# Performance work log

Hardware: AMD Instinct MI355X
Metric: run time of the kernel (lower is better)

## Reference

```python
import jax, jax.numpy as jnp
import numpy as np

NUM_GROUPS = 32
EPS = 1e-6


def setup_inputs() -> dict:
    key = jax.random.key(0)
    ks = jax.random.split(key, 6)
    b, c, H, W = 4, 512, 64, 64
    scale = 1.0 / np.sqrt(c)
    return {
        "x": jax.random.normal(ks[0], (b, c, H, W), dtype=jnp.float32),
        "gn_w": jnp.ones((c,), jnp.float32),
        "gn_b": jnp.zeros((c,), jnp.float32),
        "wq": jax.random.normal(ks[1], (c, c), jnp.float32) * scale,
        "bq": jnp.zeros((c,), jnp.float32),
        "wk": jax.random.normal(ks[2], (c, c), jnp.float32) * scale,
        "bk": jnp.zeros((c,), jnp.float32),
        "wv": jax.random.normal(ks[3], (c, c), jnp.float32) * scale,
        "bv": jnp.zeros((c,), jnp.float32),
        "wp": jax.random.normal(ks[4], (c, c), jnp.float32) * scale,
        "bp": jnp.zeros((c,), jnp.float32),
    }


def _group_norm(x, gamma, beta):
    b, c, H, W = x.shape
    xg = x.reshape(b, NUM_GROUPS, c // NUM_GROUPS, H, W)
    mean = xg.mean(axis=(2, 3, 4), keepdims=True)
    var = xg.var(axis=(2, 3, 4), keepdims=True)
    xn = (xg - mean) * jax.lax.rsqrt(var + EPS)
    xn = xn.reshape(b, c, H, W)
    return xn * gamma[None, :, None, None] + beta[None, :, None, None]


def reference(x, gn_w, gn_b, wq, bq, wk, bk, wv, bv, wp, bp):
    b, c, H, W = x.shape
    h = _group_norm(x, gn_w, gn_b)  # (b,c,H,W)
    hf = h.reshape(b, c, H * W)  # (b,c,n)
    # 1x1 convs == per-pixel linear maps; weight layout [out,in]
    q = jnp.einsum('oc,bcn->bno', wq, hf) + bq  # (b,n,c)
    k = jnp.einsum('oc,bcn->bon', wk, hf) + bk[None, :, None]  # (b,c,n)
    v = jnp.einsum('oc,bcn->bon', wv, hf) + bv[None, :, None]  # (b,c,n)
    attn = jnp.einsum('bnc,bcm->bnm', q, k) * (int(c) ** (-0.5))
    attn = jax.nn.softmax(attn, axis=2)  # softmax over keys m
    # A = v @ attn^T  -> (b,c,n) where A[:, :, n] = sum_m v[:,:,m] attn[n,m]
    A = jnp.einsum('bcm,bnm->bcn', v, attn)
    A = jnp.einsum('oc,bcn->bon', wp, A) + bp[None, :, None]
    return x + A.reshape(b, c, H, W)
```

## Files before the change

kernel.cpp:

```cpp
#include <hip/hip_runtime.h>

#define BATCH 4
#define CCH 512
#define NPIX 4096
#define NGRP 32
#define GSZ 16
#define GN_EPS 1e-6f

typedef __attribute__((ext_vector_type(8))) short short8;
typedef __attribute__((ext_vector_type(8))) unsigned short ushort8;
typedef __attribute__((ext_vector_type(4))) unsigned short ushort4v;
typedef __attribute__((ext_vector_type(4))) float f32x4;

__device__ inline unsigned short f2bf(float f) {
  unsigned u = __float_as_uint(f);
  unsigned r = u + 0x7fffu + ((u >> 16) & 1u);
  return (unsigned short)(r >> 16);
}
__device__ inline float bf2f(unsigned short us) {
  return __uint_as_float(((unsigned)us) << 16);
}

__global__ __launch_bounds__(256) void gn_stats(const float* __restrict__ x,
                                                float* __restrict__ stats) {
  int bg = blockIdx.x;
  const f32x4* base = (const f32x4*)(x + (size_t)bg * (GSZ * NPIX));
  float s = 0.f, ss = 0.f;
  const int n4 = GSZ * NPIX / 4;
  for (int i = threadIdx.x; i < n4; i += 256) {
    f32x4 v = base[i];
    s += v.x + v.y + v.z + v.w;
    ss += v.x * v.x + v.y * v.y + v.z * v.z + v.w * v.w;
  }
  for (int off = 32; off > 0; off >>= 1) {
    s += __shfl_xor(s, off, 64);
    ss += __shfl_xor(ss, off, 64);
  }
  __shared__ float rs[4], rss[4];
  int lane = threadIdx.x & 63, wid = threadIdx.x >> 6;
  if (lane == 0) { rs[wid] = s; rss[wid] = ss; }
  __syncthreads();
  if (threadIdx.x == 0) {
    float S = rs[0] + rs[1] + rs[2] + rs[3];
    float SS = rss[0] + rss[1] + rss[2] + rss[3];
    const float inv = 1.f / (float)(GSZ * NPIX);
    float mean = S * inv;
    float var = SS * inv - mean * mean;
    stats[bg * 2] = mean;
    stats[bg * 2 + 1] = rsqrtf(var + GN_EPS);
  }
}

__global__ __launch_bounds__(256) void gn_apply_t(const float* __restrict__ x,
                                                  const float* __restrict__ stats,
                                                  const float* __restrict__ gw,
                                                  const float* __restrict__ gb,
                                                  unsigned short* __restrict__ hT) {
  __shared__ float tile[64][65];
  int b = blockIdx.z, c0 = blockIdx.y * 64, n0 = blockIdx.x * 64;
  int t = threadIdx.x;
  int tc4 = t & 15, tr = t >> 4;
  const float* xb = x + ((size_t)b * CCH + c0) * NPIX + n0;
#pragma unroll
  for (int j = 0; j < 4; ++j) {
    int row = tr + j * 16;
    int c = c0 + row;
    float mean = stats[((size_t)b * NGRP + (c >> 4)) * 2];
    float rstd = stats[((size_t)b * NGRP + (c >> 4)) * 2 + 1];
    float ga = gw[c] * rstd;
    float be = gb[c] - mean * ga;
    f32x4 v = *(const f32x4*)(xb + (size_t)row * NPIX + tc4 * 4);
    tile[row][tc4 * 4 + 0] = v.x * ga + be;
    tile[row][tc4 * 4 + 1] = v.y * ga + be;
    tile[row][tc4 * 4 + 2] = v.z * ga + be;
    tile[row][tc4 * 4 + 3] = v.w * ga + be;
  }
  __syncthreads();
  int cc = t & 7, nr = t >> 3;
  unsigned short* outp = hT + ((size_t)b * NPIX + n0) * CCH + c0;
#pragma unroll
  for (int j = 0; j < 2; ++j) {
    int n = nr + j * 32;
    ushort8 pk;
#pragma unroll
    for (int i = 0; i < 8; ++i) pk[i] = f2bf(tile[cc * 8 + i][n]);
    *(ushort8*)(outp + (size_t)n * CCH + cc * 8) = pk;
  }
}

__global__ __launch_bounds__(256) void f32_to_bf16(const float* __restrict__ src,
                                                   unsigned short* __restrict__ dst,
                                                   int n4) {
  int i = blockIdx.x * 256 + threadIdx.x;
  if (i < n4) {
    f32x4 v = ((const f32x4*)src)[i];
    ushort4v o;
    o.x = f2bf(v.x); o.y = f2bf(v.y); o.z = f2bf(v.z); o.w = f2bf(v.w);
    ((ushort4v*)dst)[i] = o;
  }
}

template <int BIAS_MODE, int OUT_BF16, int RESID, int SWZ>
__global__ __launch_bounds__(256, 2) void gemm_bt(
    const unsigned short* __restrict__ A, const unsigned short* __restrict__ B,
    void* __restrict__ Cv, const float* __restrict__ bias,
    const float* __restrict__ resid, int M, int N, int K, int lda, int ldb,
    int ldc, long sA, long sB, long sC, long sR, float scale) {
  __shared__ __align__(16) unsigned short lA[128][40];
  __shared__ __align__(16) unsigned short lB[128][40];
  const int t = threadIdx.x;
  const int lane = t & 63, w = t >> 6;
  const int wr = w >> 1, wc = w & 1;
  const int fr = lane & 15, kg = lane >> 4;

  unsigned orig = blockIdx.x + gridDim.x * (blockIdx.y + gridDim.y * blockIdx.z);
  unsigned nwg = gridDim.x * gridDim.y * gridDim.z;
  unsigned tid = (orig & 7) * (nwg >> 3) + (orig >> 3);
  int mt, ntl, bz;
  if (SWZ == 2) {
    unsigned bx = tid % gridDim.x, r = tid / gridDim.x;
    ntl = (int)bx;
    mt = (int)(r % gridDim.y);
    bz = (int)(r / gridDim.y);
  } else {
    unsigned bx = tid % gridDim.x, r = tid / gridDim.x;
    mt = (int)bx;
    ntl = (int)(r % gridDim.y);
    bz = (int)(r / gridDim.y);
  }
  const int m0 = mt * 128, n0 = ntl * 128;

  const unsigned short* Abz = A + (long)bz * sA;
  const unsigned short* Bbz = B + (long)bz * sB;
  const int srow = t >> 1, skc = (t & 1) * 16;
  const unsigned short* gA = Abz + (size_t)(m0 + srow) * lda + skc;
  const unsigned short* gB = Bbz + (size_t)(n0 + srow) * ldb + skc;

  short8 a0X = *(const short8*)(gA);
  short8 a1X = *(const short8*)(gA + 8);
  short8 b0X = *(const short8*)(gB);
  short8 b1X = *(const short8*)(gB + 8);
  short8 a0Y = *(const short8*)(gA + 32);
  short8 a1Y = *(const short8*)(gA + 40);
  short8 b0Y = *(const short8*)(gB + 32);
  short8 b1Y = *(const short8*)(gB + 40);

  f32x4 acc[4][4];
  const f32x4 zero = {0.f, 0.f, 0.f, 0.f};
#pragma unroll
  for (int m = 0; m < 4; ++m)
#pragma unroll
    for (int n = 0; n < 4; ++n) acc[m][n] = zero;

  const int NT = K >> 5;
#define COMPUTE()                                                             \
  do {                                                                        \
    short8 af[4], bfr[4];                                                     \
    _Pragma("unroll") for (int m = 0; m < 4; ++m) af[m] =                     \
        *(const short8*)&lA[wr * 64 + m * 16 + fr][kg * 8];                   \
    _Pragma("unroll") for (int n = 0; n < 4; ++n) bfr[n] =                    \
        *(const short8*)&lB[wc * 64 + n * 16 + fr][kg * 8];                   \
    _Pragma("unroll") for (int m = 0; m < 4; ++m)                             \
        _Pragma("unroll") for (int n = 0; n < 4; ++n) acc[m][n] =             \
            __builtin_amdgcn_mfma_f32_16x16x32_bf16(af[m], bfr[n],            \
                                                    acc[m][n], 0, 0, 0);      \
  } while (0)

  for (int it = 0; it < NT; it += 2) {
    __syncthreads();
    *(short8*)&lA[srow][skc] = a0X;
    *(short8*)&lA[srow][skc + 8] = a1X;
    *(short8*)&lB[srow][skc] = b0X;
    *(short8*)&lB[srow][skc + 8] = b1X;
    if (it + 2 < NT) {
      a0X = *(const short8*)(gA + (it + 2) * 32);
      a1X = *(const short8*)(gA + (it + 2) * 32 + 8);
      b0X = *(const short8*)(gB + (it + 2) * 32);
      b1X = *(const short8*)(gB + (it + 2) * 32 + 8);
    }
    __syncthreads();
    COMPUTE();
    __syncthreads();
    *(short8*)&lA[srow][skc] = a0Y;
    *(short8*)&lA[srow][skc + 8] = a1Y;
    *(short8*)&lB[srow][skc] = b0Y;
    *(short8*)&lB[srow][skc + 8] = b1Y;
    if (it + 3 < NT) {
      a0Y = *(const short8*)(gA + (it + 3) * 32);
      a1Y = *(const short8*)(gA + (it + 3) * 32 + 8);
      b0Y = *(const short8*)(gB + (it + 3) * 32);
      b1Y = *(const short8*)(gB + (it + 3) * 32 + 8);
    }
    __syncthreads();
    COMPUTE();
  }
#undef COMPUTE

  const int rowbase = m0 + wr * 64 + kg * 4;
  const int colbase = n0 + wc * 64 + fr;
#pragma unroll
  for (int m = 0; m < 4; ++m) {
#pragma unroll
    for (int n = 0; n < 4; ++n) {
      int col = colbase + n * 16;
#pragma unroll
      for (int r = 0; r < 4; ++r) {
        int row = rowbase + m * 16 + r;
        float v = acc[m][n][r] * scale;
        if (BIAS_MODE == 1) v += bias[row];
        if (BIAS_MODE == 2) v += bias[col];
        if (RESID) v += resid[(size_t)bz * sR + (size_t)row * ldc + col];
        size_t idx = (size_t)bz * sC + (size_t)row * ldc + col;
        if (OUT_BF16)
          ((unsigned short*)Cv)[idx] = f2bf(v);
        else
          ((float*)Cv)[idx] = v;
      }
    }
  }
}

__global__ __launch_bounds__(512)
__attribute__((amdgpu_waves_per_eu(2, 2))) void attn_fused(
    const unsigned short* __restrict__ qg, const unsigned short* __restrict__ kgl,
    const unsigned short* __restrict__ vg, unsigned short* __restrict__ og,
    float scale) {
  __shared__ __align__(16) unsigned short Qs[64 * 512];
  __shared__ __align__(16) unsigned short Ck[2][256 * 64];
  __shared__ __align__(16) unsigned short Ps[64 * 128];

  const int t = threadIdx.x;
  const int lane = t & 63, w = t >> 6;
  const int fr = lane & 15, kgp = lane >> 4;

  unsigned logical = ((unsigned)blockIdx.x & 7) * 32 + ((unsigned)blockIdx.x >> 3);
  const int bz = (int)(logical >> 6), qt = (int)(logical & 63);
  const size_t BS = (size_t)NPIX * CCH;
  const unsigned short* qb = qg + (size_t)bz * BS + (size_t)qt * 64 * CCH;
  const unsigned short* kb = kgl + (size_t)bz * BS;
  const unsigned short* vb = vg + (size_t)bz * BS;

  const int krow = t >> 1;
  const int khalf = (t & 1) * 32;
  const int kswz = (krow & 7) << 3;

  short8 RX0, RX1, RX2, RX3, RY0, RY1, RY2, RY3;

#define LOADCH(SET, mt2, sub2)                                                \
  do {                                                                        \
    if ((mt2) < 16) {                                                         \
      const unsigned short* g;                                                \
      if ((sub2) < 8)                                                         \
        g = kb + (size_t)((mt2)*256 + krow) * CCH + (sub2)*64 + khalf;        \
      else                                                                    \
        g = vb + (size_t)t * NPIX + (mt2)*256 + ((sub2)-8) * 32;              \
      SET##0 = *(const short8*)(g);                                           \
      SET##1 = *(const short8*)(g + 8);                                       \
      SET##2 = *(const short8*)(g + 16);                                      \
      SET##3 = *(const short8*)(g + 24);                                      \
    }                                                                         \
  } while (0)

#define WRITEK(BUF, SET)                                                      \
  do {                                                                        \
    unsigned short* d = &Ck[BUF][krow * 64];                                  \
    *(short8*)(d + ((khalf + 0) ^ kswz)) = SET##0;                            \
    *(short8*)(d + ((khalf + 8) ^ kswz)) = SET##1;                            \
    *(short8*)(d + ((khalf + 16) ^ kswz)) = SET##2;                           \
    *(short8*)(d + ((khalf + 24) ^ kswz)) = SET##3;                           \
  } while (0)

#define WRITEV(BUF, SET)                                                      \
  do {                                                                        \
    unsigned short* d = &Ck[BUF][t * 8];                                      \
    *(short8*)(d + 0 * 4096) = SET##0;                                        \
    *(short8*)(d + 1 * 4096) = SET##1;                                        \
    *(short8*)(d + 2 * 4096) = SET##2;                                        \
    *(short8*)(d + 3 * 4096) = SET##3;                                        \
  } while (0)

#define PHASE_BAR()                                                           \
  do {                                                                        \
    asm volatile("s_waitcnt lgkmcnt(0)" ::: "memory");                        \
    __builtin_amdgcn_s_barrier();                                             \
    __builtin_amdgcn_sched_barrier(0);                                        \
  } while (0)

  LOADCH(RX, 0, 0);
  LOADCH(RY, 0, 1);
  {
    const int row = t >> 3, c0 = (t & 7) * 64;
    const unsigned short* src = qb + (size_t)row * CCH + c0;
    const int sw = (row & 7) << 3;
#pragma unroll
    for (int i = 0; i < 8; ++i)
      *(short8*)&Qs[row * 512 + ((c0 + i * 8) ^ sw)] = *(const short8*)(src + i * 8);
  }

  f32x4 s_acc[4][2], o_acc[4][4], racc[4];
  const f32x4 zero = {0.f, 0.f, 0.f, 0.f};
#pragma unroll
  for (int i = 0; i < 4; ++i) {
    s_acc[i][0] = zero; s_acc[i][1] = zero; racc[i] = zero;
#pragma unroll
    for (int n = 0; n < 4; ++n) o_acc[i][n] = zero;
  }

#define EXP_HALF(h)                                                           \
  do {                                                                        \
    if ((w >> 2) == (h)) {                                                    \
      _Pragma("unroll") for (int i = 0; i < 4; ++i) {                         \
        f32x4 p0, p1;                                                         \
        _Pragma("unroll") for (int r = 0; r < 4; ++r) {                       \
          p0[r] = __expf(s_acc[i][0][r] * scale);                             \
          p1[r] = __expf(s_acc[i][1][r] * scale);                             \
        }                                                                     \
        f32x4 rs = p0 + p1;                                                   \
        _Pragma("unroll") for (int off = 1; off <= 8; off <<= 1)              \
            _Pragma("unroll") for (int r = 0; r < 4; ++r) rs[r] +=            \
            __shfl_xor(rs[r], off, 64);                                       \
        racc[i] += rs;                                                        \
        _Pragma("unroll") for (int r = 0; r < 4; ++r) {                       \
          int q = i * 16 + kgp * 4 + r;                                       \
          int sw2 = (q & 7) << 3;                                             \
          Ps[q * 128 + (((w & 3) * 32 + fr) ^ sw2)] = f2bf(p0[r]);            \
          Ps[q * 128 + (((w & 3) * 32 + 16 + fr) ^ sw2)] = f2bf(p1[r]);       \
        }                                                                     \
        s_acc[i][0] = zero; s_acc[i][1] = zero;                               \
      }                                                                       \
    }                                                                         \
  } while (0)

  for (int mt = 0; mt < 16; ++mt) {
#pragma unroll
    for (int sub = 0; sub < 8; ++sub) {
      const int buf = sub & 1;
      if (buf == 0) { WRITEK(0, RX); LOADCH(RX, mt, sub + 2); }
      else          { WRITEK(1, RY); LOADCH(RY, mt, sub + 2); }
      PHASE_BAR();
      __builtin_amdgcn_s_setprio(1);
#pragma unroll
      for (int kk = 0; kk < 2; ++kk) {
        short8 a[4], b[2];
#pragma unroll
        for (int i = 0; i < 4; ++i) {
          int q = i * 16 + fr;
          a[i] = *(const short8*)&Qs[q * 512 +
                 ((sub * 64 + kk * 32 + kgp * 8) ^ ((q & 7) << 3))];
        }
#pragma unroll
        for (int n = 0; n < 2; ++n) {
          int ml = w * 32 + n * 16 + fr;
          b[n] = *(const short8*)&Ck[buf][ml * 64 +
                 ((kk * 32 + kgp * 8) ^ ((ml & 7) << 3))];
        }
#pragma unroll
        for (int i = 0; i < 4; ++i) {
          s_acc[i][0] = __builtin_amdgcn_mfma_f32_16x16x32_bf16(a[i], b[0], s_acc[i][0], 0, 0, 0);
          s_acc[i][1] = __builtin_amdgcn_mfma_f32_16x16x32_bf16(a[i], b[1], s_acc[i][1], 0, 0, 0);
        }
      }
      __builtin_amdgcn_s_setprio(0);
    }
    EXP_HALF(0);
#pragma unroll
    for (int vph = 0; vph < 8; ++vph) {
      const int sub = 8 + vph, buf = sub & 1;
      if (vph == 4) {
        PHASE_BAR();
        EXP_HALF(1);
      }
      if (buf == 0) { WRITEV(0, RX); LOADCH(RX, mt + ((sub + 2) >> 4), (sub + 2) & 15); }
      else          { WRITEV(1, RY); LOADCH(RY, mt + ((sub + 2) >> 4), (sub + 2) & 15); }
      PHASE_BAR();
      __builtin_amdgcn_s_setprio(1);
      {
        short8 a[4], b[4];
#pragma unroll
        for (int i = 0; i < 4; ++i) {
          int q = i * 16 + fr;
          a[i] = *(const short8*)&Ps[q * 128 +
                 (((vph & 3) * 32 + kgp * 8) ^ ((q & 7) << 3))];
        }
#pragma unroll
        for (int n = 0; n < 4; ++n) {
          int c = w * 64 + n * 16 + fr;
          b[n] = *(const short8*)&Ck[buf][kgp * 4096 + c * 8];
        }
#pragma unroll
        for (int i = 0; i < 4; ++i)
#pragma unroll
          for (int n = 0; n < 4; ++n)
            o_acc[i][n] = __builtin_amdgcn_mfma_f32_16x16x32_bf16(a[i], b[n], o_acc[i][n], 0, 0, 0);
      }
      __builtin_amdgcn_s_setprio(0);
    }
  }
#undef LOADCH
#undef WRITEK
#undef WRITEV
#undef EXP_HALF

  __syncthreads();
  float* lred = (float*)Ps;
  float* linv = lred + 512;
  if (fr == 0) {
#pragma unroll
    for (int i = 0; i < 4; ++i)
#pragma unroll
      for (int r = 0; r < 4; ++r)
        lred[(i * 16 + kgp * 4 + r) * 8 + w] = racc[i][r];
  }
  __syncthreads();
  if (t < 64) {
    float s = 0.f;
#pragma unroll
    for (int j = 0; j < 8; ++j) s += lred[t * 8 + j];
    linv[t] = 1.f / s;
  }
  __syncthreads();
#pragma unroll
  for (int i = 0; i < 4; ++i) {
    f32x4 li = *(const f32x4*)&linv[i * 16 + kgp * 4];
#pragma unroll
    for (int n = 0; n < 4; ++n) {
#pragma unroll
      for (int r = 0; r < 4; ++r) {
        int q = i * 16 + kgp * 4 + r;
        int col = w * 64 + n * 16 + fr;
        Qs[q * 512 + (col ^ ((q & 7) << 3))] = f2bf(o_acc[i][n][r] * li[r]);
      }
    }
  }
  __syncthreads();
  {
    const int row = t >> 3, c0 = (t & 7) * 64;
    const int sw = (row & 7) << 3;
    unsigned short* dst = og + (size_t)bz * BS + ((size_t)qt * 64 + row) * CCH + c0;
#pragma unroll
    for (int i = 0; i < 8; ++i)
      *(short8*)(dst + i * 8) = *(const short8*)&Qs[row * 512 + ((c0 + i * 8) ^ sw)];
  }
}

extern "C" void kernel_launch(void* const* d_in, const int* in_sizes, int n_in,
                              void* d_out, int out_size, void* d_ws, size_t ws_size,
                              hipStream_t stream) {
  const float* x = (const float*)d_in[0];
  const float* gnw = (const float*)d_in[1];
  const float* gnb = (const float*)d_in[2];
  const float* wq = (const float*)d_in[3];
  const float* bq = (const float*)d_in[4];
  const float* wk = (const float*)d_in[5];
  const float* bk = (const float*)d_in[6];
  const float* wv = (const float*)d_in[7];
  const float* bv = (const float*)d_in[8];
  const float* wp = (const float*)d_in[9];
  const float* bp = (const float*)d_in[10];
  float* out = (float*)d_out;

  const size_t BS = (size_t)NPIX * CCH;

  char* ws = (char*)d_ws;
  float* stats = (float*)ws;
  unsigned short* hT = (unsigned short*)(ws + 1024);
  unsigned short* Abuf = hT;
  unsigned short* qb = hT + BATCH * BS;
  unsigned short* kTb = qb + BATCH * BS;
  unsigned short* vb = kTb + BATCH * BS;
  unsigned short* wqb = vb + BATCH * BS;
  unsigned short* wkb = wqb + CCH * CCH;
  unsigned short* wvb = wkb + CCH * CCH;
  unsigned short* wpb = wvb + CCH * CCH;
  size_t need = (size_t)((char*)(wpb + CCH * CCH) - ws);
  if (ws_size < need) return;

  f32_to_bf16<<<256, 256, 0, stream>>>(wq, wqb, CCH * CCH / 4);
  f32_to_bf16<<<256, 256, 0, stream>>>(wk, wkb, CCH * CCH / 4);
  f32_to_bf16<<<256, 256, 0, stream>>>(wv, wvb, CCH * CCH / 4);
  f32_to_bf16<<<256, 256, 0, stream>>>(wp, wpb, CCH * CCH / 4);

  gn_stats<<<BATCH * NGRP, 256, 0, stream>>>(x, stats);
  gn_apply_t<<<dim3(NPIX / 64, CCH / 64, BATCH), 256, 0, stream>>>(x, stats, gnw,
                                                                   gnb, hT);

  gemm_bt<2, 1, 0, 2><<<dim3(4, 32, BATCH), 256, 0, stream>>>(
      hT, wqb, qb, bq, nullptr, NPIX, CCH, CCH, CCH, CCH, CCH, (long)BS, 0,
      (long)BS, 0, 1.f);
  gemm_bt<2, 1, 0, 2><<<dim3(4, 32, BATCH), 256, 0, stream>>>(
      hT, wkb, kTb, bk, nullptr, NPIX, CCH, CCH, CCH, CCH, CCH, (long)BS, 0,
      (long)BS, 0, 1.f);
  gemm_bt<1, 1, 0, 0><<<dim3(4, 32, BATCH), 256, 0, stream>>>(
      wvb, hT, vb, bv, nullptr, CCH, NPIX, CCH, CCH, CCH, NPIX, 0, (long)BS,
      (long)BS, 0, 1.f);

  const float sscale = 0.044194173824159216f;
  attn_fused<<<BATCH * 64, 512, 0, stream>>>(qb, kTb, vb, Abuf, sscale);

  gemm_bt<1, 0, 1, 0><<<dim3(4, 32, BATCH), 256, 0, stream>>>(
      wpb, Abuf, out, bp, x, CCH, NPIX, CCH, CCH, CCH, NPIX, 0, (long)BS,
      (long)BS, (long)BS, 1.f);
}
```

Baseline: 377.4 us.

## Stream K/V tiles directly into LDS with global_load_lds in attention

Replaces the register-staged K/V loading (global load to VGPRs, then LDS write) with direct global-to-LDS loads via the global_load_lds builtin. The source addresses are permuted so the XOR swizzle is applied at the source, and the double-buffer schedule is rewritten: the next tile is issued before compute and a vmcnt(0) barrier closes each phase. This removes the VGPR staging registers and the LDS store instructions, which may free registers and issue slots. The cost is a full vmcnt wait at every phase end, which can expose load latency, and the placement of the exp/softmax steps changes.

```diff
diff --git a/kernel.cpp b/kernel.cpp
--- a/kernel.cpp
+++ b/kernel.cpp
@@ -20,6 +20,11 @@
 __device__ inline float bf2f(unsigned short us) {
   return __uint_as_float(((unsigned)us) << 16);
 }
+
+#define GLOAD16(g, l)                                                         \
+  __builtin_amdgcn_global_load_lds(                                           \
+      (__attribute__((address_space(1))) void*)(g),                           \
+      (__attribute__((address_space(3))) void*)(l), 16, 0, 0)
 
 __global__ __launch_bounds__(256) void gn_stats(const float* __restrict__ x,
                                                 float* __restrict__ stats) {
@@ -226,7 +231,7 @@
     const unsigned short* __restrict__ vg, unsigned short* __restrict__ og,
     float scale) {
   __shared__ __align__(16) unsigned short Qs[64 * 512];
-  __shared__ __align__(16) unsigned short Ck[2][256 * 64];
+  __shared__ __align__(16) unsigned short Ck[2][16384];
   __shared__ __align__(16) unsigned short Ps[64 * 128];
 
   const int t = threadIdx.x;
@@ -240,54 +245,56 @@
   const unsigned short* kb = kgl + (size_t)bz * BS;
   const unsigned short* vb = vg + (size_t)bz * BS;
 
-  const int krow = t >> 1;
-  const int khalf = (t & 1) * 32;
-  const int kswz = (krow & 7) << 3;
-
-  short8 RX0, RX1, RX2, RX3, RY0, RY1, RY2, RY3;
-
-#define LOADCH(SET, mt2, sub2)                                                \
+  const int ldsE = w * 2048 + lane * 8;
+  const int krow_lo = lane >> 3, kg_src = (lane & 7) ^ (lane >> 3);
+  const unsigned short* kS0 = kb + (size_t)((w * 4 + 0) * 8 + krow_lo) * CCH + kg_src * 8;
+  const unsigned short* kS1 = kb + (size_t)((w * 4 + 1) * 8 + krow_lo) * CCH + kg_src * 8;
+  const unsigned short* kS2 = kb + (size_t)((w * 4 + 2) * 8 + krow_lo) * CCH + kg_src * 8;
+  const unsigned short* kS3 = kb + (size_t)((w * 4 + 3) * 8 + krow_lo) * CCH + kg_src * 8;
+#define VSRC(i) (vb + (size_t)(((w * 4 + (i)) & 7) * 64 + lane) * NPIX + ((w * 4 + (i)) >> 3) * 8)
+  const unsigned short* vS0 = VSRC(0);
+  const unsigned short* vS1 = VSRC(1);
+  const unsigned short* vS2 = VSRC(2);
+  const unsigned short* vS3 = VSRC(3);
+#undef VSRC
+
+#define ISSUE_K(BUF, mt2, sub2)                                               \
   do {                                                                        \
     if ((mt2) < 16) {                                                         \
-      const unsigned short* g;                                                \
-      if ((sub2) < 8)                                                         \
-        g = kb + (size_t)((mt2)*256 + krow) * CCH + (sub2)*64 + khalf;        \
-      else                                                                    \
-        g = vb + (size_t)t * NPIX + (mt2)*256 + ((sub2)-8) * 32;              \
-      SET##0 = *(const short8*)(g);                                           \
-      SET##1 = *(const short8*)(g + 8);                                       \
-      SET##2 = *(const short8*)(g + 16);                                      \
-      SET##3 = *(const short8*)(g + 24);                                      \
+      const long o = (long)(mt2) * (256 * CCH) + (sub2)*64;                   \
+      GLOAD16(kS0 + o, &Ck[BUF][ldsE]);                                       \
+      GLOAD16(kS1 + o, &Ck[BUF][ldsE + 512]);                                 \
+      GLOAD16(kS2 + o, &Ck[BUF][ldsE + 1024]);                                \
+      GLOAD16(kS3 + o, &Ck[BUF][ldsE + 1536]);                                \
     }                                                                         \
   } while (0)
 
-#define WRITEK(BUF, SET)                                                      \
+#define ISSUE_V(BUF, mt2, vs2)                                                \
   do {                                                                        \
-    unsigned short* d = &Ck[BUF][krow * 64];                                  \
-    *(short8*)(d + ((khalf + 0) ^ kswz)) = SET##0;                            \
-    *(short8*)(d + ((khalf + 8) ^ kswz)) = SET##1;                            \
-    *(short8*)(d + ((khalf + 16) ^ kswz)) = SET##2;                           \
-    *(short8*)(d + ((khalf + 24) ^ kswz)) = SET##3;                           \
+    if ((mt2) < 16) {                                                         \
+      const long o = (long)(mt2)*256 + (vs2)*32;                              \
+      GLOAD16(vS0 + o, &Ck[BUF][ldsE]);                                       \
+      GLOAD16(vS1 + o, &Ck[BUF][ldsE + 512]);                                 \
+      GLOAD16(vS2 + o, &Ck[BUF][ldsE + 1024]);                                \
+      GLOAD16(vS3 + o, &Ck[BUF][ldsE + 1536]);                                \
+    }                                                                         \
   } while (0)
 
-#define WRITEV(BUF, SET)                                                      \
-  do {                                                                        \
-    unsigned short* d = &Ck[BUF][t * 8];                                      \
-    *(short8*)(d + 0 * 4096) = SET##0;                                        \
-    *(short8*)(d + 1 * 4096) = SET##1;                                        \
-    *(short8*)(d + 2 * 4096) = SET##2;                                        \
-    *(short8*)(d + 3 * 4096) = SET##3;                                        \
-  } while (0)
-
-#define PHASE_BAR()                                                           \
+#define BAR_LGKM()                                                            \
   do {                                                                        \
     asm volatile("s_waitcnt lgkmcnt(0)" ::: "memory");                        \
     __builtin_amdgcn_s_barrier();                                             \
     __builtin_amdgcn_sched_barrier(0);                                        \
   } while (0)
 
-  LOADCH(RX, 0, 0);
-  LOADCH(RY, 0, 1);
+#define EXIT_BAR()                                                            \
+  do {                                                                        \
+    asm volatile("s_waitcnt vmcnt(0)" ::: "memory");                          \
+    __builtin_amdgcn_s_barrier();                                             \
+    __builtin_amdgcn_sched_barrier(0);                                        \
+  } while (0)
+
+  ISSUE_K(0, 0, 0);
   {
     const int row = t >> 3, c0 = (t & 7) * 64;
     const unsigned short* src = qb + (size_t)row * CCH + c0;
@@ -296,6 +303,7 @@
     for (int i = 0; i < 8; ++i)
       *(short8*)&Qs[row * 512 + ((c0 + i * 8) ^ sw)] = *(const short8*)(src + i * 8);
   }
+  __syncthreads();
 
   f32x4 s_acc[4][2], o_acc[4][4], racc[4];
   const f32x4 zero = {0.f, 0.f, 0.f, 0.f};
@@ -335,9 +343,9 @@
 #pragma unroll
     for (int sub = 0; sub < 8; ++sub) {
       const int buf = sub & 1;
-      if (buf == 0) { WRITEK(0, RX); LOADCH(RX, mt, sub + 2); }
-      else          { WRITEK(1, RY); LOADCH(RY, mt, sub + 2); }
-      PHASE_BAR();
+      if (sub < 7) ISSUE_K(buf ^ 1, mt, sub + 1);
+      else         ISSUE_V(buf ^ 1, mt, 0);
+      __builtin_amdgcn_sched_barrier(0);
       __builtin_amdgcn_s_setprio(1);
 #pragma unroll
       for (int kk = 0; kk < 2; ++kk) {
@@ -352,7 +360,7 @@
         for (int n = 0; n < 2; ++n) {
           int ml = w * 32 + n * 16 + fr;
           b[n] = *(const short8*)&Ck[buf][ml * 64 +
-                 ((kk * 32 + kgp * 8) ^ ((ml & 7) << 3))];
+                 (((kk * 4 + kgp) ^ (ml & 7)) << 3)];
         }
 #pragma unroll
         for (int i = 0; i < 4; ++i) {
@@ -361,18 +369,16 @@
         }
       }
       __builtin_amdgcn_s_setprio(0);
+      EXIT_BAR();
     }
-    EXP_HALF(0);
 #pragma unroll
     for (int vph = 0; vph < 8; ++vph) {
-      const int sub = 8 + vph, buf = sub & 1;
-      if (vph == 4) {
-        PHASE_BAR();
-        EXP_HALF(1);
-      }
-      if (buf == 0) { WRITEV(0, RX); LOADCH(RX, mt + ((sub + 2) >> 4), (sub + 2) & 15); }
-      else          { WRITEV(1, RY); LOADCH(RY, mt + ((sub + 2) >> 4), (sub + 2) & 15); }
-      PHASE_BAR();
+      const int buf = vph & 1;
+      if (vph < 7) ISSUE_V(buf ^ 1, mt, vph + 1);
+      else         ISSUE_K(buf ^ 1, mt + 1, 0);
+      __builtin_amdgcn_sched_barrier(0);
+      if (vph == 0) { EXP_HALF(0); BAR_LGKM(); }
+      if (vph == 4) { EXP_HALF(1); BAR_LGKM(); }
       __builtin_amdgcn_s_setprio(1);
       {
         short8 a[4], b[4];
@@ -394,12 +400,14 @@
             o_acc[i][n] = __builtin_amdgcn_mfma_f32_16x16x32_bf16(a[i], b[n], o_acc[i][n], 0, 0, 0);
       }
       __builtin_amdgcn_s_setprio(0);
+      EXIT_BAR();
     }
   }
-#undef LOADCH
-#undef WRITEK
-#undef WRITEV
+#undef ISSUE_K
+#undef ISSUE_V
 #undef EXP_HALF
+#undef BAR_LGKM
+#undef EXIT_BAR
 
   __syncthreads();
   float* lred = (float*)Ps;
```

Result: slower. 472.9 us (+25.3%).
